# Performance work log

Measured on AMD Instinct MI355X. Metric: run time of the kernel, lower is better.

Reference implementation:

```python
import jax, jax.numpy as jnp
import numpy as np

N_NODES = 50000
N_EDGES = 256000
D = 128
L = 2  # processor layers
LN_EPS = 1e-5


def _layer_norm(x, g, b):
    mu = jnp.mean(x, axis=-1, keepdims=True)
    var = jnp.mean(jnp.square(x - mu), axis=-1, keepdims=True)
    return (x - mu) * jax.lax.rsqrt(var + LN_EPS) * g + b


def _mlp(x, W1, b1, g1, be1, W2, b2):
    # Linear -> LayerNorm -> SiLU -> Linear  (num_mlp_layers=2)
    h = jax.nn.silu(_layer_norm(x @ W1 + b1, g1, be1))
    return h @ W2 + b2


def setup_inputs() -> dict:
    key = jax.random.key(0)
    ks = jax.random.split(key, 8)
    node_feat = jax.random.normal(ks[0], (N_NODES, D), dtype=jnp.float32)
    edge_attr = jax.random.normal(ks[1], (N_EDGES, D), dtype=jnp.float32)
    edge_index = jax.random.randint(ks[2], (2, N_EDGES), 0, N_NODES)
    # weights ~ N(0, 1/fan_in) per layer, stacked over L processor layers
    def w(k, shape, fan_in):
        return jax.random.normal(k, shape, dtype=jnp.float32) / np.sqrt(fan_in)
    return {
        "node_feat": node_feat,
        "edge_attr": edge_attr,
        "edge_index": edge_index,
        "e_W1": w(ks[3], (L, 3 * D, D), 3 * D),
        "e_b1": jnp.zeros((L, D), jnp.float32),
        "e_g1": jnp.ones((L, D), jnp.float32),
        "e_be1": jnp.zeros((L, D), jnp.float32),
        "e_W2": w(ks[4], (L, D, D), D),
        "e_b2": jnp.zeros((L, D), jnp.float32),
        "n_W1": w(ks[5], (L, 2 * D, D), 2 * D),
        "n_b1": jnp.zeros((L, D), jnp.float32),
        "n_g1": jnp.ones((L, D), jnp.float32),
        "n_be1": jnp.zeros((L, D), jnp.float32),
        "n_W2": w(ks[6], (L, D, D), D),
        "n_b2": jnp.zeros((L, D), jnp.float32),
    }


def reference(node_feat, edge_attr, edge_index,
              e_W1, e_b1, e_g1, e_be1, e_W2, e_b2,
              n_W1, n_b1, n_g1, n_be1, n_W2, n_b2):
    src, dst = edge_index[0], edge_index[1]
    n = node_feat
    e = edge_attr
    for i in range(L):
        # Edge block: gather src/dst node features, concat, MLP, residual
        edge_in = jnp.concatenate([e, n[src], n[dst]], axis=-1)  # [E, 3D]
        e = e + _mlp(edge_in, e_W1[i], e_b1[i], e_g1[i], e_be1[i], e_W2[i], e_b2[i])
        # Node block: scatter-add aggregate edges to dst nodes, concat, MLP, residual
        agg = jax.ops.segment_sum(e, dst, num_segments=N_NODES)  # [N, D]
        node_in = jnp.concatenate([n, agg], axis=-1)  # [N, 2D]
        n = n + _mlp(node_in, n_W1[i], n_b1[i], n_g1[i], n_be1[i], n_W2[i], n_b2[i])
    return (n, e)
```

## Files before the change

### kernel.cpp

```cpp
#include <hip/hip_runtime.h>
#include <hip/hip_bf16.h>

typedef float f32x4 __attribute__((ext_vector_type(4)));
typedef __bf16 v8bf __attribute__((ext_vector_type(8)));

#define DD 128
#define EDGES 256000
#define NODES 50000
#define SCAN_BLOCKS 49

__device__ __forceinline__ unsigned short f2bf(float f) {
    union { float f; unsigned u; } v; v.f = f;
    unsigned r = v.u + 0x7fffu + ((v.u >> 16) & 1u);
    return (unsigned short)(r >> 16);
}
__device__ __forceinline__ float bf2f(unsigned short u) {
    union { unsigned u; float f; } v; v.u = ((unsigned)u) << 16; return v.f;
}

__global__ __launch_bounds__(512)
void pack_weights(const float* __restrict__ eW1, const float* __restrict__ eW2,
                  const float* __restrict__ nW1, const float* __restrict__ nW2,
                  unsigned short* __restrict__ wp)
{
    const int b = blockIdx.x;
    const int layer = b / 24;
    const int u = b % 24;
    const int t = threadIdx.x;
    const int ct0 = t >> 6, l = t & 63;
    const int lg = l >> 4, ll = l & 15;

    if (u < 8 && u >= 4) {
        const int kt = u - 4;
        const float* W = eW1 + layer*49152;
        unsigned short* dst = wp + 32768 + layer*32768;
        #pragma unroll
        for (int h = 0; h < 2; ++h) {
            const int ct = ct0 + h*8;
            #pragma unroll
            for (int j = 0; j < 8; ++j) {
                const int k = kt*32 + lg*8 + j;
                const int cout = ct*16 + ll;
                const int row = 128 + k + ((cout >= 128) ? 128 : 0);
                const int col = cout & 127;
                dst[((kt*16 + ct)*64 + l)*8 + j] = f2bf(W[row*128 + col]);
            }
        }
        return;
    }
    const float* W; int kt; unsigned short* dst;
    if (u < 4)       { W = eW1 + layer*49152; kt = u;      dst = wp + layer*16384; }
    else if (u < 12) { W = eW2 + layer*16384; kt = u - 8;  dst = wp + 98304 + layer*16384; }
    else if (u < 20) { W = nW1 + layer*32768; kt = u - 12; dst = wp + 131072 + layer*32768; }
    else             { W = nW2 + layer*16384; kt = u - 20; dst = wp + 196608 + layer*16384; }
    #pragma unroll
    for (int j = 0; j < 8; ++j) {
        const int k = kt*32 + lg*8 + j;
        const int c = ct0*16 + ll;
        dst[((kt*8 + ct0)*64 + l)*8 + j] = f2bf(W[k*128 + c]);
    }
}

__global__ void hist_kernel(const int* __restrict__ dst, int* __restrict__ deg)
{
    const int i = blockIdx.x * blockDim.x + threadIdx.x;
    if (i < EDGES) atomicAdd(&deg[dst[i]], 1);
}

__global__ __launch_bounds__(256)
void scan_pass1(const int* __restrict__ deg, int* __restrict__ bsum)
{
    __shared__ int ws[256];
    const int b = blockIdx.x, t = threadIdx.x;
    const int base = b*1024 + t*4;
    int s = 0;
    #pragma unroll
    for (int k = 0; k < 4; ++k) {
        const int idx = base + k;
        if (idx < NODES) s += deg[idx];
    }
    ws[t] = s;
    __syncthreads();
    for (int d = 128; d >= 1; d >>= 1) {
        if (t < d) ws[t] += ws[t + d];
        __syncthreads();
    }
    if (t == 0) bsum[b] = ws[0];
}

__global__ __launch_bounds__(64)
void scan_pass2(const int* __restrict__ bsum, int* __restrict__ bbase)
{
    const int t = threadIdx.x;
    const int mine = (t < SCAN_BLOCKS) ? bsum[t] : 0;
    int v = mine;
    #pragma unroll
    for (int d = 1; d < 64; d <<= 1) {
        const int u = __shfl_up(v, d);
        if (t >= d) v += u;
    }
    if (t < SCAN_BLOCKS) bbase[t] = v - mine;
}

__global__ __launch_bounds__(256)
void scan_pass3(const int* __restrict__ deg, const int* __restrict__ bbase,
                int* __restrict__ off, int* __restrict__ cursor)
{
    __shared__ int ws[256];
    const int b = blockIdx.x, t = threadIdx.x;
    const int base = b*1024 + t*4;
    int d4[4]; int s = 0;
    #pragma unroll
    for (int k = 0; k < 4; ++k) {
        const int idx = base + k;
        d4[k] = (idx < NODES) ? deg[idx] : 0;
        s += d4[k];
    }
    ws[t] = s;
    __syncthreads();
    for (int d = 1; d < 256; d <<= 1) {
        const int u = (t >= d) ? ws[t - d] : 0;
        __syncthreads();
        ws[t] += u;
        __syncthreads();
    }
    int run = bbase[b] + ws[t] - s;
    #pragma unroll
    for (int k = 0; k < 4; ++k) {
        const int idx = base + k;
        if (idx < NODES) { off[idx] = run; cursor[idx] = run; run += d4[k]; }
    }
    if (b == 0 && t == 0) off[NODES] = EDGES;
}

__global__ void place_kernel(const int* __restrict__ dst, int* __restrict__ cursor,
                             int* __restrict__ elist)
{
    const int i = blockIdx.x * blockDim.x + threadIdx.x;
    if (i < EDGES) {
        const int p = atomicAdd(&cursor[dst[i]], 1);
        elist[p] = i;
    }
}

__global__ __launch_bounds__(256)
void node_proj(const float* __restrict__ n,
               const unsigned short* __restrict__ Wbc,
               unsigned short* __restrict__ NG)
{
    __shared__ __align__(16) unsigned short A[64][136];
    const int tid = threadIdx.x;
    const long base = (long)blockIdx.x * 64;

    #pragma unroll
    for (int it = 0; it < 8; ++it) {
        const int i = tid + it*256;
        const int row = i >> 5;
        const int c = (i & 31) * 4;
        float4 v = {0.f, 0.f, 0.f, 0.f};
        if (base + row < NODES) v = *(const float4*)&n[(base + row)*DD + c];
        ushort4 o; o.x = f2bf(v.x); o.y = f2bf(v.y); o.z = f2bf(v.z); o.w = f2bf(v.w);
        *(ushort4*)&A[row][c] = o;
    }
    __syncthreads();

    const int lane = tid & 63, w = tid >> 6;
    const int wr = w >> 1, wc = w & 1;
    const int R0 = wr*32;
    const int lg = lane >> 4, ll = lane & 15;

    f32x4 acc[2][8] = {};
    #pragma unroll
    for (int kt = 0; kt < 4; ++kt) {
        const v8bf a0 = *(const v8bf*)&A[R0 + ll][kt*32 + lg*8];
        const v8bf a1 = *(const v8bf*)&A[R0 + 16 + ll][kt*32 + lg*8];
        #pragma unroll
        for (int ct = 0; ct < 8; ++ct) {
            const v8bf b = *(const v8bf*)&Wbc[((kt*16 + wc*8 + ct)*64 + lane)*8];
            acc[0][ct] = __builtin_amdgcn_mfma_f32_16x16x32_bf16(a0, b, acc[0][ct], 0, 0, 0);
            acc[1][ct] = __builtin_amdgcn_mfma_f32_16x16x32_bf16(a1, b, acc[1][ct], 0, 0, 0);
        }
    }

    #pragma unroll
    for (int rt = 0; rt < 2; ++rt)
        #pragma unroll
        for (int j = 0; j < 4; ++j) {
            const long grow = base + R0 + rt*16 + lg*4 + j;
            if (grow < NODES) {
                ushort4 o0, o1;
                o0.x = f2bf(acc[rt][0][j]); o0.y = f2bf(acc[rt][1][j]);
                o0.z = f2bf(acc[rt][2][j]); o0.w = f2bf(acc[rt][3][j]);
                o1.x = f2bf(acc[rt][4][j]); o1.y = f2bf(acc[rt][5][j]);
                o1.z = f2bf(acc[rt][6][j]); o1.w = f2bf(acc[rt][7][j]);
                *(ushort4*)&NG[grow*256 + wc*128 + ll*4]      = o0;
                *(ushort4*)&NG[grow*256 + wc*128 + 64 + ll*4] = o1;
            }
        }
}

template <bool L0>
__global__ __launch_bounds__(256, 4)
void edge_mlp_ng(const void* __restrict__ e_in_v,
                 const unsigned short* __restrict__ NG,
                 const int* __restrict__ elist,
                 const int* __restrict__ srcA, const int* __restrict__ dstA,
                 const unsigned short* __restrict__ Wa,
                 const float* __restrict__ b1, const float* __restrict__ g1,
                 const float* __restrict__ be1,
                 const unsigned short* __restrict__ Wp2,
                 const float* __restrict__ b2,
                 unsigned short* __restrict__ ePw,
                 float* __restrict__ e_out)
{
    __shared__ __align__(16) unsigned short AeE[64][136];
    __shared__ __align__(16) unsigned short Sl[64][136];
    __shared__ float red[4][32][2];
    __shared__ int eidx[64], sidx[64], didx[64];

    const int tid = threadIdx.x;
    const long base = (long)blockIdx.x * 64;

    if (tid < 64) {
        const int i = elist[base + tid];
        eidx[tid] = i; sidx[tid] = srcA[i]; didx[tid] = dstA[i];
    }
    __syncthreads();

    const int lane = tid & 63, w = tid >> 6;
    const int wr = w >> 1, wc = w & 1;
    const int R0 = wr*32, C0 = wc*64;
    const int lg = lane >> 4, ll = lane & 15;

    ushort4 ngs[2][4], ngd[2][4];
    #pragma unroll
    for (int rt = 0; rt < 2; ++rt)
        #pragma unroll
        for (int j = 0; j < 4; ++j) {
            const int lr = rt*16 + lg*4 + j;
            const long sid = sidx[R0 + lr];
            const long did = didx[R0 + lr];
            ngs[rt][j] = *(const ushort4*)&NG[sid*256 + wc*64 + ll*4];
            ngd[rt][j] = *(const ushort4*)&NG[did*256 + 128 + wc*64 + ll*4];
        }

    if constexpr (L0) {
        const float* e_in = (const float*)e_in_v;
        #pragma unroll
        for (int it = 0; it < 8; ++it) {
            const int i = tid + it*256;
            const int row = i >> 5;
            const int c = (i & 31) * 4;
            const float4 v = *(const float4*)&e_in[(long)eidx[row]*DD + c];
            ushort4 o; o.x = f2bf(v.x); o.y = f2bf(v.y); o.z = f2bf(v.z); o.w = f2bf(v.w);
            *(ushort4*)&AeE[row][c] = o;
        }
    } else {
        const unsigned short* e_in = (const unsigned short*)e_in_v;
        #pragma unroll
        for (int it = 0; it < 4; ++it) {
            const int i = tid + it*256;
            const int row = i >> 4;
            const int c = (i & 15) * 8;
            *(uint4*)&AeE[row][c] = *(const uint4*)&e_in[(base + row)*DD + c];
        }
    }
    __syncthreads();

    float b1v[4], g1v[4], be1v[4], b2v[4];
    #pragma unroll
    for (int ct = 0; ct < 4; ++ct) {
        const int c = C0 + ct*16 + ll;
        b1v[ct] = b1[c]; g1v[ct] = g1[c]; be1v[ct] = be1[c]; b2v[ct] = b2[c];
    }

    f32x4 acc[2][4] = {};
    #pragma unroll
    for (int kt = 0; kt < 4; ++kt) {
        const v8bf a0 = *(const v8bf*)&AeE[R0 + ll][kt*32 + lg*8];
        const v8bf a1 = *(const v8bf*)&AeE[R0 + 16 + ll][kt*32 + lg*8];
        #pragma unroll
        for (int ct = 0; ct < 4; ++ct) {
            const v8bf b = *(const v8bf*)&Wa[((kt*8 + wc*4 + ct)*64 + lane)*8];
            acc[0][ct] = __builtin_amdgcn_mfma_f32_16x16x32_bf16(a0, b, acc[0][ct], 0, 0, 0);
            acc[1][ct] = __builtin_amdgcn_mfma_f32_16x16x32_bf16(a1, b, acc[1][ct], 0, 0, 0);
        }
    }

    #pragma unroll
    for (int rt = 0; rt < 2; ++rt)
        #pragma unroll
        for (int j = 0; j < 4; ++j) {
            const unsigned short* ps = (const unsigned short*)&ngs[rt][j];
            const unsigned short* pd = (const unsigned short*)&ngd[rt][j];
            #pragma unroll
            for (int ct = 0; ct < 4; ++ct)
                acc[rt][ct][j] += bf2f(ps[ct]) + bf2f(pd[ct]);
        }

    f32x4 s[2], q[2];
    #pragma unroll
    for (int rt = 0; rt < 2; ++rt) {
        #pragma unroll
        for (int ct = 0; ct < 4; ++ct) acc[rt][ct] += b1v[ct];
        s[rt] = acc[rt][0] + acc[rt][1] + acc[rt][2] + acc[rt][3];
        q[rt] = acc[rt][0]*acc[rt][0] + acc[rt][1]*acc[rt][1]
              + acc[rt][2]*acc[rt][2] + acc[rt][3]*acc[rt][3];
    }
    #pragma unroll
    for (int off = 1; off <= 8; off <<= 1) {
        #pragma unroll
        for (int rt = 0; rt < 2; ++rt)
            #pragma unroll
            for (int j = 0; j < 4; ++j) {
                s[rt][j] += __shfl_xor(s[rt][j], off);
                q[rt][j] += __shfl_xor(q[rt][j], off);
            }
    }
    if (ll == 0) {
        #pragma unroll
        for (int rt = 0; rt < 2; ++rt)
            #pragma unroll
            for (int j = 0; j < 4; ++j) {
                red[w][rt*16 + lg*4 + j][0] = s[rt][j];
                red[w][rt*16 + lg*4 + j][1] = q[rt][j];
            }
    }
    __syncthreads();

    #pragma unroll
    for (int rt = 0; rt < 2; ++rt) {
        #pragma unroll
        for (int j = 0; j < 4; ++j) {
            const int lr = rt*16 + lg*4 + j;
            const float S = red[2*wr][lr][0] + red[2*wr + 1][lr][0];
            const float Q = red[2*wr][lr][1] + red[2*wr + 1][lr][1];
            const float mu = S * (1.0f/DD);
            const float var = Q * (1.0f/DD) - mu*mu;
            const float inv = rsqrtf(var + 1e-5f);
            #pragma unroll
            for (int ct = 0; ct < 4; ++ct) {
                const float hn = (acc[rt][ct][j] - mu) * inv * g1v[ct] + be1v[ct];
                const float sv = hn / (1.0f + __expf(-hn));
                Sl[R0 + lr][C0 + ct*16 + ll] = f2bf(sv);
            }
        }
    }
    __syncthreads();

    f32x4 acc2[2][4] = {};
    #pragma unroll
    for (int kt = 0; kt < 4; ++kt) {
        const v8bf a0 = *(const v8bf*)&Sl[R0 + ll][kt*32 + lg*8];
        const v8bf a1 = *(const v8bf*)&Sl[R0 + 16 + ll][kt*32 + lg*8];
        #pragma unroll
        for (int ct = 0; ct < 4; ++ct) {
            const v8bf b = *(const v8bf*)&Wp2[((kt*8 + wc*4 + ct)*64 + lane)*8];
            acc2[0][ct] = __builtin_amdgcn_mfma_f32_16x16x32_bf16(a0, b, acc2[0][ct], 0, 0, 0);
            acc2[1][ct] = __builtin_amdgcn_mfma_f32_16x16x32_bf16(a1, b, acc2[1][ct], 0, 0, 0);
        }
    }

    #pragma unroll
    for (int rt = 0; rt < 2; ++rt)
        #pragma unroll
        for (int ct = 0; ct < 4; ++ct)
            #pragma unroll
            for (int j = 0; j < 4; ++j) {
                const int lr = rt*16 + lg*4 + j;
                const int col = C0 + ct*16 + ll;
                const float v = bf2f(AeE[R0 + lr][col]) + acc2[rt][ct][j] + b2v[ct];
                ePw[(base + R0 + lr)*DD + col] = f2bf(v);
                if constexpr (!L0)
                    e_out[(long)eidx[R0 + lr]*DD + col] = v;
            }
}

__global__ __launch_bounds__(256, 4)
void edge_mlp_full(const unsigned short* __restrict__ e_in,
                   const float* __restrict__ nf,
                   const int* __restrict__ elist,
                   const int* __restrict__ srcA, const int* __restrict__ dstA,
                   const unsigned short* __restrict__ Wa,
                   const unsigned short* __restrict__ Wbc,
                   const float* __restrict__ b1, const float* __restrict__ g1,
                   const float* __restrict__ be1,
                   const unsigned short* __restrict__ Wp2,
                   const float* __restrict__ b2, float* __restrict__ e_out)
{
    __shared__ __align__(16) unsigned short AeE[64][136];
    __shared__ __align__(16) unsigned short AeG[64][132];
    __shared__ float red[4][32][2];
    __shared__ int eidx[64], sidx[64], didx[64];

    const int tid = threadIdx.x;
    const long base = (long)blockIdx.x * 64;

    if (tid < 64) {
        const int i = elist[base + tid];
        eidx[tid] = i; sidx[tid] = srcA[i]; didx[tid] = dstA[i];
    }

    const int lane = tid & 63, w = tid >> 6;
    const int wr = w >> 1, wc = w & 1;
    const int R0 = wr*32, C0 = wc*64;
    const int lg = lane >> 4, ll = lane & 15;

    #pragma unroll
    for (int it = 0; it < 4; ++it) {
        const int i = tid + it*256;
        const int row = i >> 4;
        const int c = (i & 15) * 8;
        *(uint4*)&AeE[row][c] = *(const uint4*)&e_in[(base + row)*DD + c];
    }
    __syncthreads();

    #pragma unroll
    for (int it = 0; it < 8; ++it) {
        const int i = tid + it*256;
        const int row = i >> 5;
        const int c = (i & 31) * 4;
        const float4 v = *(const float4*)&nf[(long)sidx[row]*DD + c];
        ushort4 o; o.x = f2bf(v.x); o.y = f2bf(v.y); o.z = f2bf(v.z); o.w = f2bf(v.w);
        *(ushort4*)&AeG[row][c] = o;
    }
    float4 dreg[8];
    #pragma unroll
    for (int it = 0; it < 8; ++it) {
        const int i = tid + it*256;
        const int row = i >> 5;
        const int c = (i & 31) * 4;
        dreg[it] = *(const float4*)&nf[(long)didx[row]*DD + c];
    }
    __syncthreads();

    float b1v[4], g1v[4], be1v[4], b2v[4];
    #pragma unroll
    for (int ct = 0; ct < 4; ++ct) {
        const int c = C0 + ct*16 + ll;
        b1v[ct] = b1[c]; g1v[ct] = g1[c]; be1v[ct] = be1[c]; b2v[ct] = b2[c];
    }

    f32x4 acc[2][4] = {};
    #pragma unroll
    for (int kt = 0; kt < 8; ++kt) {
        const unsigned short* a0p = (kt < 4) ? &AeE[R0 + ll][kt*32 + lg*8]
                                             : &AeG[R0 + ll][(kt-4)*32 + lg*8];
        const unsigned short* a1p = (kt < 4) ? &AeE[R0 + 16 + ll][kt*32 + lg*8]
                                             : &AeG[R0 + 16 + ll][(kt-4)*32 + lg*8];
        const v8bf a0 = *(const v8bf*)a0p;
        const v8bf a1 = *(const v8bf*)a1p;
        #pragma unroll
        for (int ct = 0; ct < 4; ++ct) {
            const v8bf b = (kt < 4)
                ? *(const v8bf*)&Wa[((kt*8 + wc*4 + ct)*64 + lane)*8]
                : *(const v8bf*)&Wbc[(((kt-4)*16 + wc*4 + ct)*64 + lane)*8];
            acc[0][ct] = __builtin_amdgcn_mfma_f32_16x16x32_bf16(a0, b, acc[0][ct], 0, 0, 0);
            acc[1][ct] = __builtin_amdgcn_mfma_f32_16x16x32_bf16(a1, b, acc[1][ct], 0, 0, 0);
        }
    }
    __syncthreads();

    #pragma unroll
    for (int it = 0; it < 8; ++it) {
        const int i = tid + it*256;
        const int row = i >> 5;
        const int c = (i & 31) * 4;
        ushort4 o; o.x = f2bf(dreg[it].x); o.y = f2bf(dreg[it].y);
        o.z = f2bf(dreg[it].z); o.w = f2bf(dreg[it].w);
        *(ushort4*)&AeG[row][c] = o;
    }
    __syncthreads();

    #pragma unroll
    for (int kt = 0; kt < 4; ++kt) {
        const v8bf a0 = *(const v8bf*)&AeG[R0 + ll][kt*32 + lg*8];
        const v8bf a1 = *(const v8bf*)&AeG[R0 + 16 + ll][kt*32 + lg*8];
        #pragma unroll
        for (int ct = 0; ct < 4; ++ct) {
            const v8bf b = *(const v8bf*)&Wbc[((kt*16 + 8 + wc*4 + ct)*64 + lane)*8];
            acc[0][ct] = __builtin_amdgcn_mfma_f32_16x16x32_bf16(a0, b, acc[0][ct], 0, 0, 0);
            acc[1][ct] = __builtin_amdgcn_mfma_f32_16x16x32_bf16(a1, b, acc[1][ct], 0, 0, 0);
        }
    }

    f32x4 s[2], q[2];
    #pragma unroll
    for (int rt = 0; rt < 2; ++rt) {
        #pragma unroll
        for (int ct = 0; ct < 4; ++ct) acc[rt][ct] += b1v[ct];
        s[rt] = acc[rt][0] + acc[rt][1] + acc[rt][2] + acc[rt][3];
        q[rt] = acc[rt][0]*acc[rt][0] + acc[rt][1]*acc[rt][1]
              + acc[rt][2]*acc[rt][2] + acc[rt][3]*acc[rt][3];
    }
    #pragma unroll
    for (int off = 1; off <= 8; off <<= 1) {
        #pragma unroll
        for (int rt = 0; rt < 2; ++rt)
            #pragma unroll
            for (int j = 0; j < 4; ++j) {
                s[rt][j] += __shfl_xor(s[rt][j], off);
                q[rt][j] += __shfl_xor(q[rt][j], off);
            }
    }
    if (ll == 0) {
        #pragma unroll
        for (int rt = 0; rt < 2; ++rt)
            #pragma unroll
            for (int j = 0; j < 4; ++j) {
                red[w][rt*16 + lg*4 + j][0] = s[rt][j];
                red[w][rt*16 + lg*4 + j][1] = q[rt][j];
            }
    }
    __syncthreads();

    #pragma unroll
    for (int rt = 0; rt < 2; ++rt) {
        #pragma unroll
        for (int j = 0; j < 4; ++j) {
            const int lr = rt*16 + lg*4 + j;
            const float S = red[2*wr][lr][0] + red[2*wr + 1][lr][0];
            const float Q = red[2*wr][lr][1] + red[2*wr + 1][lr][1];
            const float mu = S * (1.0f/DD);
            const float var = Q * (1.0f/DD) - mu*mu;
            const float inv = rsqrtf(var + 1e-5f);
            #pragma unroll
            for (int ct = 0; ct < 4; ++ct) {
                const float hn = (acc[rt][ct][j] - mu) * inv * g1v[ct] + be1v[ct];
                const float sv = hn / (1.0f + __expf(-hn));
                AeG[R0 + lr][C0 + ct*16 + ll] = f2bf(sv);
            }
        }
    }
    __syncthreads();

    f32x4 acc2[2][4] = {};
    #pragma unroll
    for (int kt = 0; kt < 4; ++kt) {
        const v8bf a0 = *(const v8bf*)&AeG[R0 + ll][kt*32 + lg*8];
        const v8bf a1 = *(const v8bf*)&AeG[R0 + 16 + ll][kt*32 + lg*8];
        #pragma unroll
        for (int ct = 0; ct < 4; ++ct) {
            const v8bf b = *(const v8bf*)&Wp2[((kt*8 + wc*4 + ct)*64 + lane)*8];
            acc2[0][ct] = __builtin_amdgcn_mfma_f32_16x16x32_bf16(a0, b, acc2[0][ct], 0, 0, 0);
            acc2[1][ct] = __builtin_amdgcn_mfma_f32_16x16x32_bf16(a1, b, acc2[1][ct], 0, 0, 0);
        }
    }

    #pragma unroll
    for (int rt = 0; rt < 2; ++rt)
        #pragma unroll
        for (int ct = 0; ct < 4; ++ct)
            #pragma unroll
            for (int j = 0; j < 4; ++j) {
                const int lr = rt*16 + lg*4 + j;
                const int col = C0 + ct*16 + ll;
                const float v = bf2f(AeE[R0 + lr][col]) + acc2[rt][ct][j] + b2v[ct];
                e_out[(long)eidx[R0 + lr]*DD + col] = v;
            }
}

template <bool SEQ>
__global__ __launch_bounds__(256)
void node_mlp(const float* n_in, const void* __restrict__ e_buf_v,
              const int* __restrict__ off, const int* __restrict__ elist,
              const unsigned short* __restrict__ Wp1,
              const float* __restrict__ b1, const float* __restrict__ g1,
              const float* __restrict__ be1,
              const unsigned short* __restrict__ Wp2,
              const float* __restrict__ b2, float* n_out)
{
    __shared__ __align__(16) unsigned short AnN[64][136];
    __shared__ __align__(16) unsigned short AnG[64][136];
    __shared__ float red[4][32][2];

    const int tid = threadIdx.x;
    const long base = (long)blockIdx.x * 64;

    const int lane = tid & 63, w = tid >> 6;
    const int wr = w >> 1, wc = w & 1;
    const int R0 = wr*32, C0 = wc*64;
    const int lg = lane >> 4, ll = lane & 15;

    float b1v[4], g1v[4], be1v[4], b2v[4];
    #pragma unroll
    for (int ct = 0; ct < 4; ++ct) {
        const int c = C0 + ct*16 + ll;
        b1v[ct] = b1[c]; g1v[ct] = g1[c]; be1v[ct] = be1[c]; b2v[ct] = b2[c];
    }

    {
        const int r  = tid >> 2;
        const int cq = (tid & 3) * 32;
        const long row = base + r;
        float a[32];
        #pragma unroll
        for (int q = 0; q < 32; ++q) a[q] = 0.f;
        if (row < NODES) {
            const int jb = off[row], je = off[row + 1];
            for (int j = jb; j < je; ++j) {
                if constexpr (SEQ) {
                    const unsigned short* p = (const unsigned short*)e_buf_v + (long)j*DD + cq;
                    #pragma unroll
                    for (int u = 0; u < 4; ++u) {
                        const uint4 v = *(const uint4*)(p + u*8);
                        a[u*8+0] += bf2f((unsigned short)(v.x & 0xffff));
                        a[u*8+1] += bf2f((unsigned short)(v.x >> 16));
                        a[u*8+2] += bf2f((unsigned short)(v.y & 0xffff));
                        a[u*8+3] += bf2f((unsigned short)(v.y >> 16));
                        a[u*8+4] += bf2f((unsigned short)(v.z & 0xffff));
                        a[u*8+5] += bf2f((unsigned short)(v.z >> 16));
                        a[u*8+6] += bf2f((unsigned short)(v.w & 0xffff));
                        a[u*8+7] += bf2f((unsigned short)(v.w >> 16));
                    }
                } else {
                    const float* p = (const float*)e_buf_v + (long)elist[j]*DD + cq;
                    #pragma unroll
                    for (int q = 0; q < 8; ++q) {
                        const float4 v = *(const float4*)(p + q*4);
                        a[q*4+0] += v.x; a[q*4+1] += v.y;
                        a[q*4+2] += v.z; a[q*4+3] += v.w;
                    }
                }
            }
        }
        #pragma unroll
        for (int q = 0; q < 8; ++q) {
            ushort4 o;
            o.x = f2bf(a[q*4+0]); o.y = f2bf(a[q*4+1]);
            o.z = f2bf(a[q*4+2]); o.w = f2bf(a[q*4+3]);
            *(ushort4*)&AnG[r][cq + q*4] = o;
        }
    }

    #pragma unroll
    for (int it = 0; it < 8; ++it) {
        const int i = tid + it*256;
        const int row = i >> 5;
        const int c = (i & 31) * 4;
        float4 v = {0.f, 0.f, 0.f, 0.f};
        if (base + row < NODES) v = *(const float4*)&n_in[(base + row)*DD + c];
        ushort4 o; o.x = f2bf(v.x); o.y = f2bf(v.y); o.z = f2bf(v.z); o.w = f2bf(v.w);
        *(ushort4*)&AnN[row][c] = o;
    }
    __syncthreads();

    f32x4 acc[2][4] = {};
    #pragma unroll
    for (int kt = 0; kt < 8; ++kt) {
        const unsigned short* a0p = (kt < 4) ? &AnN[R0 + ll][kt*32 + lg*8]
                                             : &AnG[R0 + ll][(kt-4)*32 + lg*8];
        const unsigned short* a1p = (kt < 4) ? &AnN[R0 + 16 + ll][kt*32 + lg*8]
                                             : &AnG[R0 + 16 + ll][(kt-4)*32 + lg*8];
        const v8bf a0 = *(const v8bf*)a0p;
        const v8bf a1 = *(const v8bf*)a1p;
        #pragma unroll
        for (int ct = 0; ct < 4; ++ct) {
            const v8bf b = *(const v8bf*)&Wp1[((kt*8 + wc*4 + ct)*64 + lane)*8];
            acc[0][ct] = __builtin_amdgcn_mfma_f32_16x16x32_bf16(a0, b, acc[0][ct], 0, 0, 0);
            acc[1][ct] = __builtin_amdgcn_mfma_f32_16x16x32_bf16(a1, b, acc[1][ct], 0, 0, 0);
        }
    }

    f32x4 s[2], q2[2];
    #pragma unroll
    for (int rt = 0; rt < 2; ++rt) {
        #pragma unroll
        for (int ct = 0; ct < 4; ++ct) acc[rt][ct] += b1v[ct];
        s[rt] = acc[rt][0] + acc[rt][1] + acc[rt][2] + acc[rt][3];
        q2[rt] = acc[rt][0]*acc[rt][0] + acc[rt][1]*acc[rt][1]
               + acc[rt][2]*acc[rt][2] + acc[rt][3]*acc[rt][3];
    }
    #pragma unroll
    for (int off_ = 1; off_ <= 8; off_ <<= 1) {
        #pragma unroll
        for (int rt = 0; rt < 2; ++rt)
            #pragma unroll
            for (int j = 0; j < 4; ++j) {
                s[rt][j] += __shfl_xor(s[rt][j], off_);
                q2[rt][j] += __shfl_xor(q2[rt][j], off_);
            }
    }
    if (ll == 0) {
        #pragma unroll
        for (int rt = 0; rt < 2; ++rt)
            #pragma unroll
            for (int j = 0; j < 4; ++j) {
                red[w][rt*16 + lg*4 + j][0] = s[rt][j];
                red[w][rt*16 + lg*4 + j][1] = q2[rt][j];
            }
    }
    __syncthreads();

    #pragma unroll
    for (int rt = 0; rt < 2; ++rt) {
        #pragma unroll
        for (int j = 0; j < 4; ++j) {
            const int lr = rt*16 + lg*4 + j;
            const float S = red[2*wr][lr][0] + red[2*wr + 1][lr][0];
            const float Q = red[2*wr][lr][1] + red[2*wr + 1][lr][1];
            const float mu = S * (1.0f/DD);
            const float var = Q * (1.0f/DD) - mu*mu;
            const float inv = rsqrtf(var + 1e-5f);
            #pragma unroll
            for (int ct = 0; ct < 4; ++ct) {
                const float hn = (acc[rt][ct][j] - mu) * inv * g1v[ct] + be1v[ct];
                const float sv = hn / (1.0f + __expf(-hn));
                AnG[R0 + lr][C0 + ct*16 + ll] = f2bf(sv);
            }
        }
    }
    __syncthreads();

    f32x4 acc2[2][4] = {};
    #pragma unroll
    for (int kt = 0; kt < 4; ++kt) {
        const v8bf a0 = *(const v8bf*)&AnG[R0 + ll][kt*32 + lg*8];
        const v8bf a1 = *(const v8bf*)&AnG[R0 + 16 + ll][kt*32 + lg*8];
        #pragma unroll
        for (int ct = 0; ct < 4; ++ct) {
            const v8bf b = *(const v8bf*)&Wp2[((kt*8 + wc*4 + ct)*64 + lane)*8];
            acc2[0][ct] = __builtin_amdgcn_mfma_f32_16x16x32_bf16(a0, b, acc2[0][ct], 0, 0, 0);
            acc2[1][ct] = __builtin_amdgcn_mfma_f32_16x16x32_bf16(a1, b, acc2[1][ct], 0, 0, 0);
        }
    }

    #pragma unroll
    for (int rt = 0; rt < 2; ++rt)
        #pragma unroll
        for (int ct = 0; ct < 4; ++ct)
            #pragma unroll
            for (int j = 0; j < 4; ++j) {
                const long grow = base + R0 + rt*16 + lg*4 + j;
                if (grow < NODES) {
                    const int col = C0 + ct*16 + ll;
                    n_out[grow*DD + col] = n_in[grow*DD + col] + acc2[rt][ct][j] + b2v[ct];
                }
            }
}

extern "C" void kernel_launch(void* const* d_in, const int* in_sizes, int n_in,
                              void* d_out, int out_size, void* d_ws, size_t ws_size,
                              hipStream_t stream) {
    const float* node_feat = (const float*)d_in[0];
    const float* edge_attr = (const float*)d_in[1];
    const int*   edge_index= (const int*)d_in[2];
    const float* eW1 = (const float*)d_in[3];
    const float* eb1 = (const float*)d_in[4];
    const float* eg1 = (const float*)d_in[5];
    const float* ebe1= (const float*)d_in[6];
    const float* eW2 = (const float*)d_in[7];
    const float* eb2 = (const float*)d_in[8];
    const float* nW1 = (const float*)d_in[9];
    const float* nb1 = (const float*)d_in[10];
    const float* ng1 = (const float*)d_in[11];
    const float* nbe1= (const float*)d_in[12];
    const float* nW2 = (const float*)d_in[13];
    const float* nb2 = (const float*)d_in[14];

    const int N = NODES, E = EDGES;
    const int* src  = edge_index;
    const int* dstI = edge_index + E;

    float* out_n = (float*)d_out;
    float* out_e = (float*)d_out + (size_t)N * DD;

    unsigned short* wp = (unsigned short*)d_ws;
    int* ib     = (int*)((char*)d_ws + 458752);
    int* deg    = ib;
    int* off    = ib + 50000;
    int* cursor = ib + 100001;
    int* elist  = ib + 150001;
    int* bsum   = ib + 406001;
    int* bbase  = ib + 406065;
    unsigned short* e1w = (unsigned short*)((char*)d_ws + 2083840);
    unsigned short* NG1 = (unsigned short*)((char*)d_ws + 67619840);
    const bool big_ws = ws_size >= (67619840ull + (size_t)NODES*256*2 + 64);

    pack_weights<<<48, 512, 0, stream>>>(eW1, eW2, nW1, nW2, wp);

    hipMemsetAsync(deg, 0, (size_t)N * sizeof(int), stream);
    hist_kernel<<<(E + 255)/256, 256, 0, stream>>>(dstI, deg);
    scan_pass1<<<SCAN_BLOCKS, 256, 0, stream>>>(deg, bsum);
    scan_pass2<<<1, 64, 0, stream>>>(bsum, bbase);
    scan_pass3<<<SCAN_BLOCKS, 256, 0, stream>>>(deg, bbase, off, cursor);
    place_kernel<<<(E + 255)/256, 256, 0, stream>>>(dstI, cursor, elist);

    const int NB = (N + 63)/64;
    unsigned short* NG0 = (unsigned short*)out_e;

    node_proj<<<NB, 256, 0, stream>>>(node_feat, wp + 32768, NG0);
    edge_mlp_ng<true><<<E/64, 256, 0, stream>>>(
        edge_attr, NG0, elist, src, dstI,
        wp, eb1, eg1, ebe1, wp + 98304, eb2, e1w, nullptr);
    node_mlp<true><<<NB, 256, 0, stream>>>(
        node_feat, e1w, off, elist,
        wp + 131072, nb1, ng1, nbe1, wp + 196608, nb2, out_n);

    if (big_ws) {
        node_proj<<<NB, 256, 0, stream>>>(out_n, wp + 32768 + 32768, NG1);
        edge_mlp_ng<false><<<E/64, 256, 0, stream>>>(
            e1w, NG1, elist, src, dstI,
            wp + 16384, eb1 + DD, eg1 + DD, ebe1 + DD,
            wp + 98304 + 16384, eb2 + DD, e1w , out_e);
        node_mlp<true><<<NB, 256, 0, stream>>>(
            out_n, e1w, off, elist,
            wp + 131072 + 32768, nb1 + DD, ng1 + DD, nbe1 + DD,
            wp + 196608 + 16384, nb2 + DD, out_n);
    } else {
        edge_mlp_full<<<E/64, 256, 0, stream>>>(
            e1w, out_n, elist, src, dstI,
            wp + 16384, wp + 32768 + 32768,
            eb1 + DD, eg1 + DD, ebe1 + DD,
            wp + 98304 + 16384, eb2 + DD, out_e);
        node_mlp<false><<<NB, 256, 0, stream>>>(
            out_n, out_e, off, elist,
            wp + 131072 + 32768, nb1 + DD, ng1 + DD, nbe1 + DD,
            wp + 196608 + 16384, nb2 + DD, out_n);
    }
}
```

Before: 354.3 us.

## Make edge MLP wave-independent with full-width rows and pre-permuted src/dst

The edge MLP kernel now gives each wave 16 full rows across all 128 output columns. That removes the cross-wave LayerNorm reduction through shared memory and every block-level __syncthreads, which become wave barriers. A new perm_kernel builds src/dst arrays in sorted edge order, so each wave loads its indices as int4 instead of through a shared-memory indirection. In exchange each wave carries 8 accumulator tiles (more registers), the extra permutation pass costs memory traffic, and the workspace offsets move.

```diff
diff --git a/kernel.cpp b/kernel.cpp
--- a/kernel.cpp
+++ b/kernel.cpp
@@ -140,6 +140,18 @@
     if (i < EDGES) {
         const int p = atomicAdd(&cursor[dst[i]], 1);
         elist[p] = i;
+    }
+}
+
+__global__ void perm_kernel(const int* __restrict__ elist,
+                            const int* __restrict__ srcA, const int* __restrict__ dstA,
+                            int* __restrict__ srcP, int* __restrict__ dstP)
+{
+    const int i = blockIdx.x * blockDim.x + threadIdx.x;
+    if (i < EDGES) {
+        const int e = elist[i];
+        srcP[i] = srcA[e];
+        dstP[i] = dstA[e];
     }
 }
 
@@ -203,8 +215,8 @@
 __global__ __launch_bounds__(256, 4)
 void edge_mlp_ng(const void* __restrict__ e_in_v,
                  const unsigned short* __restrict__ NG,
-                 const int* __restrict__ elist,
-                 const int* __restrict__ srcA, const int* __restrict__ dstA,
+                 const int* __restrict__ eidxP,
+                 const int* __restrict__ srcP, const int* __restrict__ dstP,
                  const unsigned short* __restrict__ Wa,
                  const float* __restrict__ b1, const float* __restrict__ g1,
                  const float* __restrict__ be1,
@@ -213,167 +225,143 @@
                  unsigned short* __restrict__ ePw,
                  float* __restrict__ e_out)
 {
-    __shared__ __align__(16) unsigned short AeE[64][136];
-    __shared__ __align__(16) unsigned short Sl[64][136];
-    __shared__ float red[4][32][2];
-    __shared__ int eidx[64], sidx[64], didx[64];
+    __shared__ __align__(16) unsigned short AeE[4][16][136];
+    __shared__ __align__(16) unsigned short Sl[4][16][136];
 
     const int tid = threadIdx.x;
-    const long base = (long)blockIdx.x * 64;
-
-    if (tid < 64) {
-        const int i = elist[base + tid];
-        eidx[tid] = i; sidx[tid] = srcA[i]; didx[tid] = dstA[i];
-    }
-    __syncthreads();
-
-    const int lane = tid & 63, w = tid >> 6;
-    const int wr = w >> 1, wc = w & 1;
-    const int R0 = wr*32, C0 = wc*64;
+    const int wv = tid >> 6, lane = tid & 63;
     const int lg = lane >> 4, ll = lane & 15;
-
-    ushort4 ngs[2][4], ngd[2][4];
-    #pragma unroll
-    for (int rt = 0; rt < 2; ++rt)
-        #pragma unroll
-        for (int j = 0; j < 4; ++j) {
-            const int lr = rt*16 + lg*4 + j;
-            const long sid = sidx[R0 + lr];
-            const long did = didx[R0 + lr];
-            ngs[rt][j] = *(const ushort4*)&NG[sid*256 + wc*64 + ll*4];
-            ngd[rt][j] = *(const ushort4*)&NG[did*256 + 128 + wc*64 + ll*4];
-        }
+    const long rb = (long)blockIdx.x * 64 + wv * 16;
+
+    unsigned short (*Ae)[136] = AeE[wv];
+    unsigned short (*Sw)[136] = Sl[wv];
+
+    const int4 s4 = *(const int4*)&srcP[rb + lg*4];
+    const int4 d4 = *(const int4*)&dstP[rb + lg*4];
+    const int sid[4] = {s4.x, s4.y, s4.z, s4.w};
+    const int did[4] = {d4.x, d4.y, d4.z, d4.w};
+
+    ushort4 ngsl[4], ngsh[4], ngdl[4], ngdh[4];
+    #pragma unroll
+    for (int j = 0; j < 4; ++j) {
+        const unsigned short* ps = NG + (long)sid[j]*256 + ll*4;
+        const unsigned short* pd = NG + (long)did[j]*256 + 128 + ll*4;
+        ngsl[j] = *(const ushort4*)(ps);
+        ngsh[j] = *(const ushort4*)(ps + 64);
+        ngdl[j] = *(const ushort4*)(pd);
+        ngdh[j] = *(const ushort4*)(pd + 64);
+    }
 
     if constexpr (L0) {
         const float* e_in = (const float*)e_in_v;
         #pragma unroll
         for (int it = 0; it < 8; ++it) {
-            const int i = tid + it*256;
+            const int i = it*64 + lane;
             const int row = i >> 5;
             const int c = (i & 31) * 4;
-            const float4 v = *(const float4*)&e_in[(long)eidx[row]*DD + c];
+            const int eidx = eidxP[rb + row];
+            const float4 v = *(const float4*)&e_in[(long)eidx*DD + c];
             ushort4 o; o.x = f2bf(v.x); o.y = f2bf(v.y); o.z = f2bf(v.z); o.w = f2bf(v.w);
-            *(ushort4*)&AeE[row][c] = o;
+            *(ushort4*)&Ae[row][c] = o;
         }
     } else {
         const unsigned short* e_in = (const unsigned short*)e_in_v;
         #pragma unroll
         for (int it = 0; it < 4; ++it) {
-            const int i = tid + it*256;
+            const int i = it*64 + lane;
             const int row = i >> 4;
             const int c = (i & 15) * 8;
-            *(uint4*)&AeE[row][c] = *(const uint4*)&e_in[(base + row)*DD + c];
-        }
-    }
-    __syncthreads();
-
-    float b1v[4], g1v[4], be1v[4], b2v[4];
-    #pragma unroll
-    for (int ct = 0; ct < 4; ++ct) {
-        const int c = C0 + ct*16 + ll;
-        b1v[ct] = b1[c]; g1v[ct] = g1[c]; be1v[ct] = be1[c]; b2v[ct] = b2[c];
-    }
-
-    f32x4 acc[2][4] = {};
+            *(uint4*)&Ae[row][c] = *(const uint4*)&e_in[(rb + row)*DD + c];
+        }
+    }
+    __builtin_amdgcn_wave_barrier();
+
+    f32x4 acc[8] = {};
     #pragma unroll
     for (int kt = 0; kt < 4; ++kt) {
-        const v8bf a0 = *(const v8bf*)&AeE[R0 + ll][kt*32 + lg*8];
-        const v8bf a1 = *(const v8bf*)&AeE[R0 + 16 + ll][kt*32 + lg*8];
-        #pragma unroll
-        for (int ct = 0; ct < 4; ++ct) {
-            const v8bf b = *(const v8bf*)&Wa[((kt*8 + wc*4 + ct)*64 + lane)*8];
-            acc[0][ct] = __builtin_amdgcn_mfma_f32_16x16x32_bf16(a0, b, acc[0][ct], 0, 0, 0);
-            acc[1][ct] = __builtin_amdgcn_mfma_f32_16x16x32_bf16(a1, b, acc[1][ct], 0, 0, 0);
-        }
-    }
-
-    #pragma unroll
-    for (int rt = 0; rt < 2; ++rt)
+        const v8bf a0 = *(const v8bf*)&Ae[ll][kt*32 + lg*8];
+        #pragma unroll
+        for (int ct = 0; ct < 8; ++ct) {
+            const v8bf b = *(const v8bf*)&Wa[((kt*8 + ct)*64 + lane)*8];
+            acc[ct] = __builtin_amdgcn_mfma_f32_16x16x32_bf16(a0, b, acc[ct], 0, 0, 0);
+        }
+    }
+
+    #pragma unroll
+    for (int j = 0; j < 4; ++j) {
+        const unsigned short* sl = (const unsigned short*)&ngsl[j];
+        const unsigned short* sh = (const unsigned short*)&ngsh[j];
+        const unsigned short* dl = (const unsigned short*)&ngdl[j];
+        const unsigned short* dh = (const unsigned short*)&ngdh[j];
+        #pragma unroll
+        for (int c4 = 0; c4 < 4; ++c4) {
+            acc[c4][j]     += bf2f(sl[c4]) + bf2f(dl[c4]);
+            acc[4 + c4][j] += bf2f(sh[c4]) + bf2f(dh[c4]);
+        }
+    }
+
+    float g1v[8], be1v[8];
+    #pragma unroll
+    for (int ct = 0; ct < 8; ++ct) {
+        const int c = ct*16 + ll;
+        acc[ct] += b1[c];
+        g1v[ct] = g1[c]; be1v[ct] = be1[c];
+    }
+    f32x4 s = acc[0] + acc[1] + acc[2] + acc[3] + acc[4] + acc[5] + acc[6] + acc[7];
+    f32x4 q = acc[0]*acc[0] + acc[1]*acc[1] + acc[2]*acc[2] + acc[3]*acc[3]
+            + acc[4]*acc[4] + acc[5]*acc[5] + acc[6]*acc[6] + acc[7]*acc[7];
+    #pragma unroll
+    for (int off = 1; off <= 8; off <<= 1) {
         #pragma unroll
         for (int j = 0; j < 4; ++j) {
-            const unsigned short* ps = (const unsigned short*)&ngs[rt][j];
-            const unsigned short* pd = (const unsigned short*)&ngd[rt][j];
-            #pragma unroll
-            for (int ct = 0; ct < 4; ++ct)
-                acc[rt][ct][j] += bf2f(ps[ct]) + bf2f(pd[ct]);
-        }
-
-    f32x4 s[2], q[2];
-    #pragma unroll
-    for (int rt = 0; rt < 2; ++rt) {
-        #pragma unroll
-        for (int ct = 0; ct < 4; ++ct) acc[rt][ct] += b1v[ct];
-        s[rt] = acc[rt][0] + acc[rt][1] + acc[rt][2] + acc[rt][3];
-        q[rt] = acc[rt][0]*acc[rt][0] + acc[rt][1]*acc[rt][1]
-              + acc[rt][2]*acc[rt][2] + acc[rt][3]*acc[rt][3];
-    }
-    #pragma unroll
-    for (int off = 1; off <= 8; off <<= 1) {
-        #pragma unroll
-        for (int rt = 0; rt < 2; ++rt)
-            #pragma unroll
-            for (int j = 0; j < 4; ++j) {
-                s[rt][j] += __shfl_xor(s[rt][j], off);
-                q[rt][j] += __shfl_xor(q[rt][j], off);
-            }
-    }
-    if (ll == 0) {
-        #pragma unroll
-        for (int rt = 0; rt < 2; ++rt)
-            #pragma unroll
-            for (int j = 0; j < 4; ++j) {
-                red[w][rt*16 + lg*4 + j][0] = s[rt][j];
-                red[w][rt*16 + lg*4 + j][1] = q[rt][j];
-            }
-    }
-    __syncthreads();
-
-    #pragma unroll
-    for (int rt = 0; rt < 2; ++rt) {
+            s[j] += __shfl_xor(s[j], off);
+            q[j] += __shfl_xor(q[j], off);
+        }
+    }
+
+    #pragma unroll
+    for (int j = 0; j < 4; ++j) {
+        const float mu = s[j] * (1.0f/DD);
+        const float var = q[j] * (1.0f/DD) - mu*mu;
+        const float inv = rsqrtf(var + 1e-5f);
+        #pragma unroll
+        for (int ct = 0; ct < 8; ++ct) {
+            const float hn = (acc[ct][j] - mu) * inv * g1v[ct] + be1v[ct];
+            const float sv = hn / (1.0f + __expf(-hn));
+            Sw[lg*4 + j][ct*16 + ll] = f2bf(sv);
+        }
+    }
+    __builtin_amdgcn_wave_barrier();
+
+    f32x4 acc2[8] = {};
+    #pragma unroll
+    for (int kt = 0; kt < 4; ++kt) {
+        const v8bf a0 = *(const v8bf*)&Sw[ll][kt*32 + lg*8];
+        #pragma unroll
+        for (int ct = 0; ct < 8; ++ct) {
+            const v8bf b = *(const v8bf*)&Wp2[((kt*8 + ct)*64 + lane)*8];
+            acc2[ct] = __builtin_amdgcn_mfma_f32_16x16x32_bf16(a0, b, acc2[ct], 0, 0, 0);
+        }
+    }
+
+    int eid[4] = {0, 0, 0, 0};
+    if constexpr (!L0) {
+        const int4 e4 = *(const int4*)&eidxP[rb + lg*4];
+        eid[0] = e4.x; eid[1] = e4.y; eid[2] = e4.z; eid[3] = e4.w;
+    }
+    #pragma unroll
+    for (int ct = 0; ct < 8; ++ct) {
+        const int col = ct*16 + ll;
+        const float b2v = b2[col];
         #pragma unroll
         for (int j = 0; j < 4; ++j) {
-            const int lr = rt*16 + lg*4 + j;
-            const float S = red[2*wr][lr][0] + red[2*wr + 1][lr][0];
-            const float Q = red[2*wr][lr][1] + red[2*wr + 1][lr][1];
-            const float mu = S * (1.0f/DD);
-            const float var = Q * (1.0f/DD) - mu*mu;
-            const float inv = rsqrtf(var + 1e-5f);
-            #pragma unroll
-            for (int ct = 0; ct < 4; ++ct) {
-                const float hn = (acc[rt][ct][j] - mu) * inv * g1v[ct] + be1v[ct];
-                const float sv = hn / (1.0f + __expf(-hn));
-                Sl[R0 + lr][C0 + ct*16 + ll] = f2bf(sv);
-            }
-        }
-    }
-    __syncthreads();
-
-    f32x4 acc2[2][4] = {};
-    #pragma unroll
-    for (int kt = 0; kt < 4; ++kt) {
-        const v8bf a0 = *(const v8bf*)&Sl[R0 + ll][kt*32 + lg*8];
-        const v8bf a1 = *(const v8bf*)&Sl[R0 + 16 + ll][kt*32 + lg*8];
-        #pragma unroll
-        for (int ct = 0; ct < 4; ++ct) {
-            const v8bf b = *(const v8bf*)&Wp2[((kt*8 + wc*4 + ct)*64 + lane)*8];
-            acc2[0][ct] = __builtin_amdgcn_mfma_f32_16x16x32_bf16(a0, b, acc2[0][ct], 0, 0, 0);
-            acc2[1][ct] = __builtin_amdgcn_mfma_f32_16x16x32_bf16(a1, b, acc2[1][ct], 0, 0, 0);
-        }
-    }
-
-    #pragma unroll
-    for (int rt = 0; rt < 2; ++rt)
-        #pragma unroll
-        for (int ct = 0; ct < 4; ++ct)
-            #pragma unroll
-            for (int j = 0; j < 4; ++j) {
-                const int lr = rt*16 + lg*4 + j;
-                const int col = C0 + ct*16 + ll;
-                const float v = bf2f(AeE[R0 + lr][col]) + acc2[rt][ct][j] + b2v[ct];
-                ePw[(base + R0 + lr)*DD + col] = f2bf(v);
-                if constexpr (!L0)
-                    e_out[(long)eidx[R0 + lr]*DD + col] = v;
-            }
+            const int row = lg*4 + j;
+            const float v = bf2f(Ae[row][col]) + acc2[ct][j] + b2v;
+            ePw[(rb + row)*DD + col] = f2bf(v);
+            if constexpr (!L0)
+                e_out[(long)eid[j]*DD + col] = v;
+        }
+    }
 }
 
 __global__ __launch_bounds__(256, 4)
@@ -770,12 +758,14 @@
     int* deg    = ib;
     int* off    = ib + 50000;
     int* cursor = ib + 100001;
-    int* elist  = ib + 150001;
-    int* bsum   = ib + 406001;
-    int* bbase  = ib + 406065;
-    unsigned short* e1w = (unsigned short*)((char*)d_ws + 2083840);
-    unsigned short* NG1 = (unsigned short*)((char*)d_ws + 67619840);
-    const bool big_ws = ws_size >= (67619840ull + (size_t)NODES*256*2 + 64);
+    int* elist  = ib + 150004;
+    int* srcP   = ib + 406004;
+    int* dstP   = ib + 662004;
+    int* bsum   = ib + 918004;
+    int* bbase  = ib + 918068;
+    unsigned short* e1w = (unsigned short*)((char*)d_ws + 4131328);
+    unsigned short* NG1 = (unsigned short*)((char*)d_ws + 69667328);
+    const bool big_ws = ws_size >= (69667328ull + (size_t)NODES*256*2 + 64);
 
     pack_weights<<<48, 512, 0, stream>>>(eW1, eW2, nW1, nW2, wp);
 
@@ -785,13 +775,14 @@
     scan_pass2<<<1, 64, 0, stream>>>(bsum, bbase);
     scan_pass3<<<SCAN_BLOCKS, 256, 0, stream>>>(deg, bbase, off, cursor);
     place_kernel<<<(E + 255)/256, 256, 0, stream>>>(dstI, cursor, elist);
+    perm_kernel<<<(E + 255)/256, 256, 0, stream>>>(elist, src, dstI, srcP, dstP);
 
     const int NB = (N + 63)/64;
     unsigned short* NG0 = (unsigned short*)out_e;
 
     node_proj<<<NB, 256, 0, stream>>>(node_feat, wp + 32768, NG0);
     edge_mlp_ng<true><<<E/64, 256, 0, stream>>>(
-        edge_attr, NG0, elist, src, dstI,
+        edge_attr, NG0, elist, srcP, dstP,
         wp, eb1, eg1, ebe1, wp + 98304, eb2, e1w, nullptr);
     node_mlp<true><<<NB, 256, 0, stream>>>(
         node_feat, e1w, off, elist,
@@ -800,7 +791,7 @@
     if (big_ws) {
         node_proj<<<NB, 256, 0, stream>>>(out_n, wp + 32768 + 32768, NG1);
         edge_mlp_ng<false><<<E/64, 256, 0, stream>>>(
-            e1w, NG1, elist, src, dstI,
+            e1w, NG1, elist, srcP, dstP,
             wp + 16384, eb1 + DD, eg1 + DD, ebe1 + DD,
             wp + 98304 + 16384, eb2 + DD, e1w , out_e);
         node_mlp<true><<<NB, 256, 0, stream>>>(
```

Result: no change. 355.5 us (+0.3%).
